# Kernel tuning notes

Hardware: AMD Instinct MI355X
Metric: run time of the kernel (lower is better)

The kernel has to match this reference:

```python
import jax, jax.numpy as jnp
import numpy as np

B, S, T = 4, 1024, 1024
CTX, QIN, C, H = 1024, 1024, 1024, 16
HD = C // H  # per-head channels


def setup_inputs() -> dict:
    key = jax.random.key(0)
    ks = jax.random.split(key, 12)
    s = 0.02
    return {
        "query": jax.random.normal(ks[0], (B, S, QIN), jnp.float32),
        "key": jax.random.normal(ks[1], (B, T, CTX), jnp.float32),
        "value": jax.random.normal(ks[2], (B, T, CTX), jnp.float32),
        "mask": jax.random.randint(ks[3], (B, S, T), 0, 2).astype(bool),
        "Wq": jax.random.normal(ks[4], (C, QIN), jnp.float32) * s,
        "bq": jax.random.normal(ks[5], (C,), jnp.float32) * s,
        "Wk": jax.random.normal(ks[6], (C, CTX), jnp.float32) * s,
        "bk": jax.random.normal(ks[7], (C,), jnp.float32) * s,
        "Wv": jax.random.normal(ks[8], (C, CTX), jnp.float32) * s,
        "bv": jax.random.normal(ks[9], (C,), jnp.float32) * s,
        "Wo": jax.random.normal(ks[10], (C, C), jnp.float32) * s,
        "bo": jax.random.normal(ks[11], (C,), jnp.float32) * s,
    }


def reference(query, key, value, mask, Wq, bq, Wk, bk, Wv, bv, Wo, bo):
    b, s, _ = query.shape
    t = key.shape[1]
    c = Wq.shape[0]
    h, hd = H, c // H
    q = (query @ Wq.T + bq).reshape(b, s, h, hd)
    k = (key @ Wk.T + bk).reshape(b, t, h, hd)
    v = (value @ Wv.T + bv).reshape(b, t, h, hd)
    # [B,H,S,T] scores, scaled by 1/sqrt(head_dim)
    score = jnp.einsum('bshd,bthd->bhst', q, k) * (hd ** -0.5)
    # masked_fill_(~mask[:, None, 0:1], -inf): mask key positions via row 0
    score = jnp.where(mask[:, None, 0:1], score, -jnp.inf)
    weights = jax.nn.softmax(score, axis=-1)
    out = jnp.einsum('bhst,bthd->bshd', weights, v).reshape(b, s, c)
    out = out @ Wo.T + bo
    out = out * mask[..., 0:1].astype(out.dtype)
    return out
```

## Files before the change

### kernel.cpp

```cpp
#include <hip/hip_runtime.h>
#include <stdint.h>

#define Bb  4
#define Ss  1024
#define Tt  1024
#define Cc  1024
#define Hh  16
#define HDd 64
#define Kk  1024

typedef __bf16 bf16;
typedef __bf16 bf16x8 __attribute__((ext_vector_type(8)));
typedef float  f32x4  __attribute__((ext_vector_type(4)));
typedef __attribute__((address_space(1))) uint32_t gu32;
typedef __attribute__((address_space(3))) uint32_t lu32;

__device__ __forceinline__ void load_lds16(const bf16* g, bf16* l) {
    __builtin_amdgcn_global_load_lds((gu32*)g, (lu32*)l, 16, 0, 0);
}

__global__ void cvt8(const float* __restrict__ s0, const float* __restrict__ s1,
                     const float* __restrict__ s2, const float* __restrict__ s3,
                     bf16* __restrict__ d0, bf16* __restrict__ d1,
                     bf16* __restrict__ d2, bf16* __restrict__ d3, int n)
{
    const float* s; bf16* d;
    switch (blockIdx.y) {
        case 0: s = s0; d = d0; break;
        case 1: s = s1; d = d1; break;
        case 2: s = s2; d = d2; break;
        default: s = s3; d = d3; break;
    }
    const int i = (blockIdx.x * blockDim.x + threadIdx.x) * 8;
    if (i >= n) return;
    const float4 a = *(const float4*)(s + i);
    const float4 c = *(const float4*)(s + i + 4);
    bf16x8 o;
    o[0] = (bf16)a.x; o[1] = (bf16)a.y; o[2] = (bf16)a.z; o[3] = (bf16)a.w;
    o[4] = (bf16)c.x; o[5] = (bf16)c.y; o[6] = (bf16)c.z; o[7] = (bf16)c.w;
    *(bf16x8*)(d + i) = o;
}

__device__ __forceinline__ void gemm_mainloop(
    const bf16* __restrict__ A, const bf16* __restrict__ W,
    bf16* As, bf16* Bs, f32x4 acc[4][4])
{
    const int tid  = threadIdx.x;
    const int wid  = tid >> 6;
    const int lane = tid & 63;
    const int l16  = lane & 15;
    const int quad = lane >> 4;
    const int wm   = wid >> 1;
    const int wn   = wid & 1;
    const int lr   = lane >> 2;
    const int lc   = (lane & 3) * 8;
    const bf16* Ab = A + (size_t)blockIdx.x * 128 * Kk;
    const bf16* Wb = W + (size_t)blockIdx.y * 128 * Kk;

    for (int k0 = 0; k0 < Kk; k0 += 32) {
#pragma unroll
        for (int p = 0; p < 2; p++) {
            const int r0 = wid * 32 + p * 16;
            load_lds16(Ab + (size_t)(r0 + lr) * Kk + k0 + lc, As + r0 * 32);
            load_lds16(Wb + (size_t)(r0 + lr) * Kk + k0 + lc, Bs + r0 * 32);
        }
        __syncthreads();
        bf16x8 af[4], bw[4];
#pragma unroll
        for (int i = 0; i < 4; i++)
            af[i] = *(const bf16x8*)(As + (wm * 64 + i * 16 + l16) * 32 + quad * 8);
#pragma unroll
        for (int j = 0; j < 4; j++)
            bw[j] = *(const bf16x8*)(Bs + (wn * 64 + j * 16 + l16) * 32 + quad * 8);
#pragma unroll
        for (int i = 0; i < 4; i++)
#pragma unroll
            for (int j = 0; j < 4; j++)
                acc[i][j] = __builtin_amdgcn_mfma_f32_16x16x32_bf16(af[i], bw[j], acc[i][j], 0, 0, 0);
        __syncthreads();
    }
}

__global__ __launch_bounds__(256)
void gemm_qkv(const bf16* __restrict__ Aq, const bf16* __restrict__ Ak, const bf16* __restrict__ Av,
              const bf16* __restrict__ Wq, const bf16* __restrict__ Wk, const bf16* __restrict__ Wv,
              const float* __restrict__ bq, const float* __restrict__ bk, const float* __restrict__ bv,
              bf16* __restrict__ Oq, bf16* __restrict__ Ok, bf16* __restrict__ Ov)
{
    __shared__ __align__(16) bf16 As[128 * 32];
    __shared__ __align__(16) bf16 Bs[128 * 32];
    const int z = blockIdx.z;
    const bf16*  A    = (z == 0) ? Aq : (z == 1) ? Ak : Av;
    const bf16*  W    = (z == 0) ? Wq : (z == 1) ? Wk : Wv;
    const float* bias = (z == 0) ? bq : (z == 1) ? bk : bv;
    bf16*        O    = (z == 0) ? Oq : (z == 1) ? Ok : Ov;

    f32x4 acc[4][4];
    const f32x4 z4 = {0.f, 0.f, 0.f, 0.f};
#pragma unroll
    for (int i = 0; i < 4; i++)
#pragma unroll
        for (int j = 0; j < 4; j++) acc[i][j] = z4;

    gemm_mainloop(A, W, As, Bs, acc);

    const int tid = threadIdx.x;
    const int wid = tid >> 6, lane = tid & 63;
    const int l16 = lane & 15, quad = lane >> 4;
    const int wm = wid >> 1, wn = wid & 1;
    const int row0 = blockIdx.x * 128 + wm * 64;
    const int col0 = blockIdx.y * 128 + wn * 64;
#pragma unroll
    for (int j = 0; j < 4; j++) {
        const int col = col0 + j * 16 + l16;
        const float bj = bias[col];
        const int h = col >> 6, d = col & 63;
#pragma unroll
        for (int i = 0; i < 4; i++) {
#pragma unroll
            for (int r = 0; r < 4; r++) {
                const int row = row0 + i * 16 + quad * 4 + r;
                const int b = row >> 10, s = row & 1023;
                const bf16 val = (bf16)(acc[i][j][r] + bj);
                if (z == 2) {
                    Ov[((size_t)((b * Hh + h) * HDd + d)) * Tt + s] = val;
                } else {
                    O[((size_t)(b * Hh + h) * Ss + s) * HDd + d] = val;
                }
            }
        }
    }
}

__global__ __launch_bounds__(256)
void gemm_out(const bf16* __restrict__ A, const bf16* __restrict__ W,
              const float* __restrict__ bias, const int* __restrict__ mask,
              float* __restrict__ out)
{
    __shared__ __align__(16) bf16 As[128 * 32];
    __shared__ __align__(16) bf16 Bs[128 * 32];
    f32x4 acc[4][4];
    const f32x4 z4 = {0.f, 0.f, 0.f, 0.f};
#pragma unroll
    for (int i = 0; i < 4; i++)
#pragma unroll
        for (int j = 0; j < 4; j++) acc[i][j] = z4;

    gemm_mainloop(A, W, As, Bs, acc);

    const int tid = threadIdx.x;
    const int wid = tid >> 6, lane = tid & 63;
    const int l16 = lane & 15, quad = lane >> 4;
    const int wm = wid >> 1, wn = wid & 1;
    const int row0 = blockIdx.x * 128 + wm * 64;
    const int col0 = blockIdx.y * 128 + wn * 64;
#pragma unroll
    for (int j = 0; j < 4; j++) {
        const int col = col0 + j * 16 + l16;
        const float bj = bias[col];
#pragma unroll
        for (int i = 0; i < 4; i++) {
#pragma unroll
            for (int r = 0; r < 4; r++) {
                const int row = row0 + i * 16 + quad * 4 + r;
                const float mval = (mask[(size_t)row * Tt] != 0) ? 1.f : 0.f;
                out[(size_t)row * Cc + col] = (acc[i][j][r] + bj) * mval;
            }
        }
    }
}

__global__ __launch_bounds__(256)
void attn(const bf16* __restrict__ Q, const bf16* __restrict__ Kp, const bf16* __restrict__ Vt,
          const int* __restrict__ mask, bf16* __restrict__ X)
{
    __shared__ __align__(16) bf16 Ks[64 * 64];
    __shared__ __align__(16) bf16 Vs[64 * 64];
    __shared__ __align__(16) bf16 Ps[4][16 * 72];
    const int bh = blockIdx.y;
    const int b = bh >> 4, h = bh & 15;
    const int tid = threadIdx.x, wid = tid >> 6, lane = tid & 63;
    const int l16 = lane & 15, quad = lane >> 4;
    const bf16* Qbh = Q  + (size_t)bh * Ss * HDd;
    const bf16* Kbh = Kp + (size_t)bh * Tt * HDd;
    const bf16* Vbh = Vt + (size_t)bh * HDd * Tt;
    const int*  mb  = mask + (size_t)b * Ss * Tt;
    const int q0 = blockIdx.x * 64 + wid * 16;
    bf16* Psw = &Ps[wid][0];

    const bf16x8 qf0 = *(const bf16x8*)(Qbh + (size_t)(q0 + l16) * HDd + quad * 8);
    const bf16x8 qf1 = *(const bf16x8*)(Qbh + (size_t)(q0 + l16) * HDd + 32 + quad * 8);

    float ls[4];
    f32x4 o[4];
    const f32x4 z4 = {0.f, 0.f, 0.f, 0.f};
#pragma unroll
    for (int r = 0; r < 4; r++) ls[r] = 0.f;
#pragma unroll
    for (int dblk = 0; dblk < 4; dblk++) o[dblk] = z4;

    const int srow = lane >> 3;
    const int schk = lane & 7;
    const int sswz = (schk ^ srow) * 8;

    for (int kt = 0; kt < Tt; kt += 64) {
#pragma unroll
        for (int p = 0; p < 2; p++) {
            const int c8 = wid * 2 + p;
            load_lds16(Kbh + (size_t)(kt + c8 * 8 + srow) * HDd + sswz,
                       Ks + c8 * 512);
            load_lds16(Vbh + (size_t)(c8 * 8 + srow) * Tt + kt + sswz,
                       Vs + c8 * 512);
        }
        __syncthreads();

        f32x4 sc[4];
#pragma unroll
        for (int nb = 0; nb < 4; nb++) sc[nb] = z4;
#pragma unroll
        for (int nb = 0; nb < 4; nb++) {
            const bf16* krow = Ks + (nb * 16 + l16) * 64;
            const bf16x8 kf0 = *(const bf16x8*)(krow + ((quad     ^ (l16 & 7)) * 8));
            const bf16x8 kf1 = *(const bf16x8*)(krow + (((4 + quad) ^ (l16 & 7)) * 8));
            sc[nb] = __builtin_amdgcn_mfma_f32_16x16x32_bf16(qf0, kf0, sc[nb], 0, 0, 0);
            sc[nb] = __builtin_amdgcn_mfma_f32_16x16x32_bf16(qf1, kf1, sc[nb], 0, 0, 0);
        }

#pragma unroll
        for (int nb = 0; nb < 4; nb++) {
            const float madd = mb[kt + nb * 16 + l16] ? 0.f : -1e30f;
#pragma unroll
            for (int r = 0; r < 4; r++) {
                const float p = __expf(sc[nb][r] * 0.125f + madd);
                ls[r] += p;
                Psw[(quad * 4 + r) * 72 + nb * 16 + l16] = (bf16)p;
            }
        }

#pragma unroll
        for (int kh = 0; kh < 2; kh++) {
            const bf16x8 pf = *(const bf16x8*)(Psw + l16 * 72 + kh * 32 + quad * 8);
#pragma unroll
            for (int dblk = 0; dblk < 4; dblk++) {
                const bf16x8 vf = *(const bf16x8*)(Vs + (dblk * 16 + l16) * 64 +
                                                   (((kh * 4 + quad) ^ (l16 & 7)) * 8));
                o[dblk] = __builtin_amdgcn_mfma_f32_16x16x32_bf16(pf, vf, o[dblk], 0, 0, 0);
            }
        }
        __syncthreads();
    }

#pragma unroll
    for (int off = 1; off <= 8; off <<= 1)
#pragma unroll
        for (int r = 0; r < 4; r++)
            ls[r] += __shfl_xor(ls[r], off, 64);
    float inv[4];
#pragma unroll
    for (int r = 0; r < 4; r++) inv[r] = 1.f / ls[r];

#pragma unroll
    for (int dblk = 0; dblk < 4; dblk++) {
#pragma unroll
        for (int r = 0; r < 4; r++) {
            const int srow_q = q0 + quad * 4 + r;
            const int d = dblk * 16 + l16;
            X[(size_t)(b * Ss + srow_q) * Cc + h * HDd + d] = (bf16)(o[dblk][r] * inv[r]);
        }
    }
}

extern "C" void kernel_launch(void* const* d_in, const int* in_sizes, int n_in,
                              void* d_out, int out_size, void* d_ws, size_t ws_size,
                              hipStream_t stream)
{
    const float* query = (const float*)d_in[0];
    const float* key   = (const float*)d_in[1];
    const float* value = (const float*)d_in[2];
    const int*   mask  = (const int*)d_in[3];
    const float* Wq = (const float*)d_in[4];
    const float* bq = (const float*)d_in[5];
    const float* Wk = (const float*)d_in[6];
    const float* bk = (const float*)d_in[7];
    const float* Wv = (const float*)d_in[8];
    const float* bv = (const float*)d_in[9];
    const float* Wo = (const float*)d_in[10];
    const float* bo = (const float*)d_in[11];
    float* out = (float*)d_out;

    char* ws = (char*)d_ws;
    const size_t MB = 1024 * 1024;
    bf16* qb  = (bf16*)(ws + 0 * MB);
    bf16* kb  = (bf16*)(ws + 8 * MB);
    bf16* vb  = (bf16*)(ws + 16 * MB);
    bf16* wqb = (bf16*)(ws + 24 * MB);
    bf16* wkb = (bf16*)(ws + 26 * MB);
    bf16* wvb = (bf16*)(ws + 28 * MB);
    bf16* wob = (bf16*)(ws + 30 * MB);
    bf16* Qp  = (bf16*)(ws + 32 * MB);
    bf16* Kpp = (bf16*)(ws + 40 * MB);
    bf16* Vtp = (bf16*)(ws + 48 * MB);
    bf16* Xb  = (bf16*)(ws + 56 * MB);

    cvt8<<<dim3(2048, 3), 256, 0, stream>>>(query, key, value, query,
                                            qb, kb, vb, qb, Bb * Ss * Kk);
    cvt8<<<dim3(512, 4), 256, 0, stream>>>(Wq, Wk, Wv, Wo,
                                           wqb, wkb, wvb, wob, Cc * Kk);
    gemm_qkv<<<dim3(32, 8, 3), 256, 0, stream>>>(qb, kb, vb, wqb, wkb, wvb,
                                                 bq, bk, bv, Qp, Kpp, Vtp);
    attn<<<dim3(16, 64), 256, 0, stream>>>(Qp, Kpp, Vtp, mask, Xb);
    gemm_out<<<dim3(32, 8), 256, 0, stream>>>(Xb, wob, bo, mask, out);
}
```

Baseline: 240.2 us.

## Split attention over key ranges per wave with per-wave pipelined staging and LDS reduction

The attention kernel now gives each wave a 256-key slice of the sequence for all 64 queries of the block, instead of giving each wave 16 queries over all keys. Each wave double-issues its own K/V tile loads into private LDS and uses waitcnt instead of block-wide barriers, so the per-tile __syncthreads goes away. Partial outputs and row sums are combined through LDS at the end, and the results are written as vectorised stores. Softmax uses exp2 with a folded scale, and the mask is hoisted into registers. The two conversion launches are merged into one. Risks are heavier register pressure from 16 accumulator tiles, a large LDS footprint that limits occupancy, and loss of the intra-wave K/V reuse across waves.

```diff
diff --git a/kernel.cpp b/kernel.cpp
--- a/kernel.cpp
+++ b/kernel.cpp
@@ -21,15 +21,22 @@
 
 __global__ void cvt8(const float* __restrict__ s0, const float* __restrict__ s1,
                      const float* __restrict__ s2, const float* __restrict__ s3,
+                     const float* __restrict__ s4, const float* __restrict__ s5,
+                     const float* __restrict__ s6,
                      bf16* __restrict__ d0, bf16* __restrict__ d1,
-                     bf16* __restrict__ d2, bf16* __restrict__ d3, int n)
-{
-    const float* s; bf16* d;
+                     bf16* __restrict__ d2, bf16* __restrict__ d3,
+                     bf16* __restrict__ d4, bf16* __restrict__ d5,
+                     bf16* __restrict__ d6)
+{
+    const float* s; bf16* d; int n;
     switch (blockIdx.y) {
-        case 0: s = s0; d = d0; break;
-        case 1: s = s1; d = d1; break;
-        case 2: s = s2; d = d2; break;
-        default: s = s3; d = d3; break;
+        case 0: s = s0; d = d0; n = Bb * Ss * Kk; break;
+        case 1: s = s1; d = d1; n = Bb * Ss * Kk; break;
+        case 2: s = s2; d = d2; n = Bb * Ss * Kk; break;
+        case 3: s = s3; d = d3; n = Cc * Kk; break;
+        case 4: s = s4; d = d4; n = Cc * Kk; break;
+        case 5: s = s5; d = d5; n = Cc * Kk; break;
+        default: s = s6; d = d6; n = Cc * Kk; break;
     }
     const int i = (blockIdx.x * blockDim.x + threadIdx.x) * 8;
     if (i >= n) return;
@@ -170,104 +177,169 @@
     }
 }
 
-__global__ __launch_bounds__(256)
+#define WAITVM0()   asm volatile("s_waitcnt vmcnt(0)" ::: "memory")
+#define WAITLGKM0() asm volatile("s_waitcnt lgkmcnt(0)" ::: "memory")
+
+__global__ __launch_bounds__(256, 2)
 void attn(const bf16* __restrict__ Q, const bf16* __restrict__ Kp, const bf16* __restrict__ Vt,
           const int* __restrict__ mask, bf16* __restrict__ X)
 {
-    __shared__ __align__(16) bf16 Ks[64 * 64];
-    __shared__ __align__(16) bf16 Vs[64 * 64];
-    __shared__ __align__(16) bf16 Ps[4][16 * 72];
+    __shared__ __align__(16) char smem_raw[70656];
+    bf16* smem = (bf16*)smem_raw;
     const int bh = blockIdx.y;
     const int b = bh >> 4, h = bh & 15;
     const int tid = threadIdx.x, wid = tid >> 6, lane = tid & 63;
     const int l16 = lane & 15, quad = lane >> 4;
-    const bf16* Qbh = Q  + (size_t)bh * Ss * HDd;
-    const bf16* Kbh = Kp + (size_t)bh * Tt * HDd;
-    const bf16* Vbh = Vt + (size_t)bh * HDd * Tt;
-    const int*  mb  = mask + (size_t)b * Ss * Tt;
-    const int q0 = blockIdx.x * 64 + wid * 16;
-    bf16* Psw = &Ps[wid][0];
-
-    const bf16x8 qf0 = *(const bf16x8*)(Qbh + (size_t)(q0 + l16) * HDd + quad * 8);
-    const bf16x8 qf1 = *(const bf16x8*)(Qbh + (size_t)(q0 + l16) * HDd + 32 + quad * 8);
-
-    float ls[4];
-    f32x4 o[4];
+    const int q0 = blockIdx.x * 64;
+
+    const bf16* Qbh  = Q  + (size_t)bh * Ss * HDd;
+    const bf16* KbhW = Kp + (size_t)bh * Tt * HDd + (size_t)(wid * 256) * HDd;
+    const bf16* VbhW = Vt + (size_t)bh * HDd * Tt + wid * 256;
+    const int*  mbW  = mask + (size_t)b * Ss * Tt + wid * 256;
+
+    bf16* wslot = smem + wid * 5376;
+    bf16* kb = wslot;
+    bf16* vb = wslot + 2048;
+    bf16* Pbuf[2] = { wslot + 4096, wslot + 4736 };
+
+    const int r8  = lane >> 3;
+    const int sw8 = ((lane & 7) ^ (r8 & 7)) * 8;
+    const int r4  = lane >> 2;
+    const int sw4 = ((lane & 3) ^ (r4 & 3)) * 8;
+
+#define STAGE(ii) do { \
+    _Pragma("unroll") \
+    for (int c = 0; c < 4; ++c) \
+        load_lds16(KbhW + (size_t)((ii) * 32 + c * 8 + r8) * HDd + sw8, kb + c * 512); \
+    _Pragma("unroll") \
+    for (int c = 0; c < 4; ++c) \
+        load_lds16(VbhW + (size_t)(c * 16 + r4) * Tt + (ii) * 32 + sw4, vb + c * 512); \
+} while (0)
+
+    bf16x8 qf[4][2];
+#pragma unroll
+    for (int mi = 0; mi < 4; ++mi)
+#pragma unroll
+        for (int kh = 0; kh < 2; ++kh)
+            qf[mi][kh] = *(const bf16x8*)(Qbh + (size_t)(q0 + mi * 16 + l16) * HDd + kh * 32 + quad * 8);
+
+    float madd[16];
+#pragma unroll
+    for (int j = 0; j < 16; ++j)
+        madd[j] = mbW[j * 16 + l16] ? 0.f : -1e30f;
+
     const f32x4 z4 = {0.f, 0.f, 0.f, 0.f};
-#pragma unroll
-    for (int r = 0; r < 4; r++) ls[r] = 0.f;
-#pragma unroll
-    for (int dblk = 0; dblk < 4; dblk++) o[dblk] = z4;
-
-    const int srow = lane >> 3;
-    const int schk = lane & 7;
-    const int sswz = (schk ^ srow) * 8;
-
-    for (int kt = 0; kt < Tt; kt += 64) {
-#pragma unroll
-        for (int p = 0; p < 2; p++) {
-            const int c8 = wid * 2 + p;
-            load_lds16(Kbh + (size_t)(kt + c8 * 8 + srow) * HDd + sswz,
-                       Ks + c8 * 512);
-            load_lds16(Vbh + (size_t)(c8 * 8 + srow) * Tt + kt + sswz,
-                       Vs + c8 * 512);
+    f32x4 o[4][4];
+    float ls[4][4];
+#pragma unroll
+    for (int mi = 0; mi < 4; ++mi) {
+#pragma unroll
+        for (int dblk = 0; dblk < 4; ++dblk) o[mi][dblk] = z4;
+#pragma unroll
+        for (int r = 0; r < 4; ++r) ls[mi][r] = 0.f;
+    }
+
+    const float C2 = 0.18033688f;
+
+    STAGE(0);
+#pragma unroll
+    for (int i = 0; i < 8; ++i) {
+        WAITVM0();
+        bf16x8 kf[2][2], vf[4];
+#pragma unroll
+        for (int nb = 0; nb < 2; ++nb)
+#pragma unroll
+            for (int kh = 0; kh < 2; ++kh)
+                kf[nb][kh] = *(const bf16x8*)(kb + (nb * 16 + l16) * 64 +
+                                              (((kh * 4 + quad) ^ (l16 & 7)) * 8));
+#pragma unroll
+        for (int dblk = 0; dblk < 4; ++dblk)
+            vf[dblk] = *(const bf16x8*)(vb + (dblk * 16 + l16) * 32 +
+                                        ((quad ^ (l16 & 3)) * 8));
+        WAITLGKM0();
+        if (i < 7) STAGE(i + 1);
+
+#define QKEXP(mi, pb) do { \
+    f32x4 s0 = z4, s1 = z4; \
+    s0 = __builtin_amdgcn_mfma_f32_16x16x32_bf16(qf[mi][0], kf[0][0], s0, 0, 0, 0); \
+    s0 = __builtin_amdgcn_mfma_f32_16x16x32_bf16(qf[mi][1], kf[0][1], s0, 0, 0, 0); \
+    s1 = __builtin_amdgcn_mfma_f32_16x16x32_bf16(qf[mi][0], kf[1][0], s1, 0, 0, 0); \
+    s1 = __builtin_amdgcn_mfma_f32_16x16x32_bf16(qf[mi][1], kf[1][1], s1, 0, 0, 0); \
+    _Pragma("unroll") \
+    for (int r = 0; r < 4; ++r) { \
+        const float p0 = exp2f(s0[r] * C2 + madd[i * 2 + 0]); \
+        const float p1 = exp2f(s1[r] * C2 + madd[i * 2 + 1]); \
+        ls[mi][r] += p0 + p1; \
+        (pb)[(quad * 4 + r) * 40 + l16]      = (bf16)p0; \
+        (pb)[(quad * 4 + r) * 40 + 16 + l16] = (bf16)p1; \
+    } \
+} while (0)
+
+        QKEXP(0, Pbuf[0]);
+#pragma unroll
+        for (int mi = 0; mi < 4; ++mi) {
+            if (mi == 0) QKEXP(1, Pbuf[1]);
+            if (mi == 1) QKEXP(2, Pbuf[0]);
+            if (mi == 2) QKEXP(3, Pbuf[1]);
+            const bf16x8 pf = *(const bf16x8*)(Pbuf[mi & 1] + l16 * 40 + quad * 8);
+#pragma unroll
+            for (int dblk = 0; dblk < 4; ++dblk)
+                o[mi][dblk] = __builtin_amdgcn_mfma_f32_16x16x32_bf16(pf, vf[dblk], o[mi][dblk], 0, 0, 0);
         }
-        __syncthreads();
-
-        f32x4 sc[4];
-#pragma unroll
-        for (int nb = 0; nb < 4; nb++) sc[nb] = z4;
-#pragma unroll
-        for (int nb = 0; nb < 4; nb++) {
-            const bf16* krow = Ks + (nb * 16 + l16) * 64;
-            const bf16x8 kf0 = *(const bf16x8*)(krow + ((quad     ^ (l16 & 7)) * 8));
-            const bf16x8 kf1 = *(const bf16x8*)(krow + (((4 + quad) ^ (l16 & 7)) * 8));
-            sc[nb] = __builtin_amdgcn_mfma_f32_16x16x32_bf16(qf0, kf0, sc[nb], 0, 0, 0);
-            sc[nb] = __builtin_amdgcn_mfma_f32_16x16x32_bf16(qf1, kf1, sc[nb], 0, 0, 0);
-        }
-
-#pragma unroll
-        for (int nb = 0; nb < 4; nb++) {
-            const float madd = mb[kt + nb * 16 + l16] ? 0.f : -1e30f;
-#pragma unroll
-            for (int r = 0; r < 4; r++) {
-                const float p = __expf(sc[nb][r] * 0.125f + madd);
-                ls[r] += p;
-                Psw[(quad * 4 + r) * 72 + nb * 16 + l16] = (bf16)p;
-            }
-        }
-
-#pragma unroll
-        for (int kh = 0; kh < 2; kh++) {
-            const bf16x8 pf = *(const bf16x8*)(Psw + l16 * 72 + kh * 32 + quad * 8);
-#pragma unroll
-            for (int dblk = 0; dblk < 4; dblk++) {
-                const bf16x8 vf = *(const bf16x8*)(Vs + (dblk * 16 + l16) * 64 +
-                                                   (((kh * 4 + quad) ^ (l16 & 7)) * 8));
-                o[dblk] = __builtin_amdgcn_mfma_f32_16x16x32_bf16(pf, vf, o[dblk], 0, 0, 0);
-            }
-        }
-        __syncthreads();
-    }
+#undef QKEXP
+    }
+#undef STAGE
 
 #pragma unroll
     for (int off = 1; off <= 8; off <<= 1)
 #pragma unroll
-        for (int r = 0; r < 4; r++)
-            ls[r] += __shfl_xor(ls[r], off, 64);
-    float inv[4];
-#pragma unroll
-    for (int r = 0; r < 4; r++) inv[r] = 1.f / ls[r];
-
-#pragma unroll
-    for (int dblk = 0; dblk < 4; dblk++) {
-#pragma unroll
-        for (int r = 0; r < 4; r++) {
-            const int srow_q = q0 + quad * 4 + r;
-            const int d = dblk * 16 + l16;
-            X[(size_t)(b * Ss + srow_q) * Cc + h * HDd + d] = (bf16)(o[dblk][r] * inv[r]);
-        }
-    }
+        for (int mi = 0; mi < 4; ++mi)
+#pragma unroll
+            for (int r = 0; r < 4; ++r)
+                ls[mi][r] += __shfl_xor(ls[mi][r], off, 64);
+
+    __syncthreads();
+    float* Om = (float*)smem + wid * 4416;
+#pragma unroll
+    for (int mi = 0; mi < 4; ++mi)
+#pragma unroll
+        for (int dblk = 0; dblk < 4; ++dblk)
+#pragma unroll
+            for (int r = 0; r < 4; ++r)
+                Om[(mi * 16 + quad * 4 + r) * 68 + dblk * 16 + l16] = o[mi][dblk][r];
+    if (l16 == 0) {
+#pragma unroll
+        for (int mi = 0; mi < 4; ++mi)
+#pragma unroll
+            for (int r = 0; r < 4; ++r)
+                Om[4352 + mi * 16 + quad * 4 + r] = ls[mi][r];
+    }
+    __syncthreads();
+
+    const int rl = wid * 16 + l16;
+    f32x4 a[4] = { z4, z4, z4, z4 };
+    float lt = 0.f;
+#pragma unroll
+    for (int u = 0; u < 4; ++u) {
+        const float* Ou = (const float*)smem + u * 4416;
+#pragma unroll
+        for (int e = 0; e < 4; ++e)
+            a[e] += *(const f32x4*)(Ou + rl * 68 + quad * 16 + e * 4);
+        lt += Ou[4352 + rl];
+    }
+    const float inv = 1.f / lt;
+
+    bf16x8 w0, w1;
+#pragma unroll
+    for (int c = 0; c < 4; ++c) {
+        w0[c]     = (bf16)(a[0][c] * inv);
+        w0[4 + c] = (bf16)(a[1][c] * inv);
+        w1[c]     = (bf16)(a[2][c] * inv);
+        w1[4 + c] = (bf16)(a[3][c] * inv);
+    }
+    bf16* Xrow = X + (size_t)(b * Ss + q0 + rl) * Cc + h * HDd + quad * 16;
+    *(bf16x8*)(Xrow)     = w0;
+    *(bf16x8*)(Xrow + 8) = w1;
 }
 
 extern "C" void kernel_launch(void* const* d_in, const int* in_sizes, int n_in,
@@ -302,10 +374,8 @@
     bf16* Vtp = (bf16*)(ws + 48 * MB);
     bf16* Xb  = (bf16*)(ws + 56 * MB);
 
-    cvt8<<<dim3(2048, 3), 256, 0, stream>>>(query, key, value, query,
-                                            qb, kb, vb, qb, Bb * Ss * Kk);
-    cvt8<<<dim3(512, 4), 256, 0, stream>>>(Wq, Wk, Wv, Wo,
-                                           wqb, wkb, wvb, wob, Cc * Kk);
+    cvt8<<<dim3(2048, 7), 256, 0, stream>>>(query, key, value, Wq, Wk, Wv, Wo,
+                                            qb, kb, vb, wqb, wkb, wvb, wob);
     gemm_qkv<<<dim3(32, 8, 3), 256, 0, stream>>>(qb, kb, vb, wqb, wkb, wvb,
                                                  bq, bk, bv, Qp, Kpp, Vtp);
     attn<<<dim3(16, 64), 256, 0, stream>>>(Qp, Kpp, Vtp, mask, Xb);
```

Measured after the change: 264.9 us. 1.1x slower.

## Double-buffer K/V tiles in attention and merge conversion launches

Applied to the files above, without the earlier changes.

The attention kernel now keeps two LDS buffers for its K and V tiles. It issues the async global-to-LDS load for the next tile right after a single barrier, so the copy overlaps with the current tile's MFMA and softmax work, and the trailing barrier is dropped. The two fp32-to-bf16 conversion launches are merged into one grid with seven slices, each carrying its own length. This saves a kernel launch, but the weight slices launch many blocks that exit immediately, and the doubled LDS use may lower occupancy.

```diff
diff --git a/kernel.cpp b/kernel.cpp
--- a/kernel.cpp
+++ b/kernel.cpp
@@ -21,15 +21,22 @@
 
 __global__ void cvt8(const float* __restrict__ s0, const float* __restrict__ s1,
                      const float* __restrict__ s2, const float* __restrict__ s3,
+                     const float* __restrict__ s4, const float* __restrict__ s5,
+                     const float* __restrict__ s6,
                      bf16* __restrict__ d0, bf16* __restrict__ d1,
-                     bf16* __restrict__ d2, bf16* __restrict__ d3, int n)
-{
-    const float* s; bf16* d;
+                     bf16* __restrict__ d2, bf16* __restrict__ d3,
+                     bf16* __restrict__ d4, bf16* __restrict__ d5,
+                     bf16* __restrict__ d6)
+{
+    const float* s; bf16* d; int n;
     switch (blockIdx.y) {
-        case 0: s = s0; d = d0; break;
-        case 1: s = s1; d = d1; break;
-        case 2: s = s2; d = d2; break;
-        default: s = s3; d = d3; break;
+        case 0: s = s0; d = d0; n = Bb * Ss * Kk; break;
+        case 1: s = s1; d = d1; n = Bb * Ss * Kk; break;
+        case 2: s = s2; d = d2; n = Bb * Ss * Kk; break;
+        case 3: s = s3; d = d3; n = Cc * Kk; break;
+        case 4: s = s4; d = d4; n = Cc * Kk; break;
+        case 5: s = s5; d = d5; n = Cc * Kk; break;
+        default: s = s6; d = d6; n = Cc * Kk; break;
     }
     const int i = (blockIdx.x * blockDim.x + threadIdx.x) * 8;
     if (i >= n) return;
@@ -174,8 +181,8 @@
 void attn(const bf16* __restrict__ Q, const bf16* __restrict__ Kp, const bf16* __restrict__ Vt,
           const int* __restrict__ mask, bf16* __restrict__ X)
 {
-    __shared__ __align__(16) bf16 Ks[64 * 64];
-    __shared__ __align__(16) bf16 Vs[64 * 64];
+    __shared__ __align__(16) bf16 Ks[2][64 * 64];
+    __shared__ __align__(16) bf16 Vs[2][64 * 64];
     __shared__ __align__(16) bf16 Ps[4][16 * 72];
     const int bh = blockIdx.y;
     const int b = bh >> 4, h = bh & 15;
@@ -203,24 +210,31 @@
     const int schk = lane & 7;
     const int sswz = (schk ^ srow) * 8;
 
-    for (int kt = 0; kt < Tt; kt += 64) {
-#pragma unroll
-        for (int p = 0; p < 2; p++) {
-            const int c8 = wid * 2 + p;
-            load_lds16(Kbh + (size_t)(kt + c8 * 8 + srow) * HDd + sswz,
-                       Ks + c8 * 512);
-            load_lds16(Vbh + (size_t)(c8 * 8 + srow) * Tt + kt + sswz,
-                       Vs + c8 * 512);
-        }
+#define STAGE(it, buf) do { \
+    _Pragma("unroll") \
+    for (int p = 0; p < 2; p++) { \
+        const int c8 = wid * 2 + p; \
+        load_lds16(Kbh + (size_t)((it) * 64 + c8 * 8 + srow) * HDd + sswz, \
+                   Ks[buf] + c8 * 512); \
+        load_lds16(Vbh + (size_t)(c8 * 8 + srow) * Tt + (it) * 64 + sswz, \
+                   Vs[buf] + c8 * 512); \
+    } \
+} while (0)
+
+    STAGE(0, 0);
+    for (int it = 0; it < 16; ++it) {
+        const int cur = it & 1;
+        const int kt = it * 64;
         __syncthreads();
+        if (it < 15) STAGE(it + 1, cur ^ 1);
 
         f32x4 sc[4];
 #pragma unroll
         for (int nb = 0; nb < 4; nb++) sc[nb] = z4;
 #pragma unroll
         for (int nb = 0; nb < 4; nb++) {
-            const bf16* krow = Ks + (nb * 16 + l16) * 64;
-            const bf16x8 kf0 = *(const bf16x8*)(krow + ((quad     ^ (l16 & 7)) * 8));
+            const bf16* krow = Ks[cur] + (nb * 16 + l16) * 64;
+            const bf16x8 kf0 = *(const bf16x8*)(krow + ((quad       ^ (l16 & 7)) * 8));
             const bf16x8 kf1 = *(const bf16x8*)(krow + (((4 + quad) ^ (l16 & 7)) * 8));
             sc[nb] = __builtin_amdgcn_mfma_f32_16x16x32_bf16(qf0, kf0, sc[nb], 0, 0, 0);
             sc[nb] = __builtin_amdgcn_mfma_f32_16x16x32_bf16(qf1, kf1, sc[nb], 0, 0, 0);
@@ -242,13 +256,13 @@
             const bf16x8 pf = *(const bf16x8*)(Psw + l16 * 72 + kh * 32 + quad * 8);
 #pragma unroll
             for (int dblk = 0; dblk < 4; dblk++) {
-                const bf16x8 vf = *(const bf16x8*)(Vs + (dblk * 16 + l16) * 64 +
+                const bf16x8 vf = *(const bf16x8*)(Vs[cur] + (dblk * 16 + l16) * 64 +
                                                    (((kh * 4 + quad) ^ (l16 & 7)) * 8));
                 o[dblk] = __builtin_amdgcn_mfma_f32_16x16x32_bf16(pf, vf, o[dblk], 0, 0, 0);
             }
         }
-        __syncthreads();
-    }
+    }
+#undef STAGE
 
 #pragma unroll
     for (int off = 1; off <= 8; off <<= 1)
@@ -302,10 +316,8 @@
     bf16* Vtp = (bf16*)(ws + 48 * MB);
     bf16* Xb  = (bf16*)(ws + 56 * MB);
 
-    cvt8<<<dim3(2048, 3), 256, 0, stream>>>(query, key, value, query,
-                                            qb, kb, vb, qb, Bb * Ss * Kk);
-    cvt8<<<dim3(512, 4), 256, 0, stream>>>(Wq, Wk, Wv, Wo,
-                                           wqb, wkb, wvb, wob, Cc * Kk);
+    cvt8<<<dim3(2048, 7), 256, 0, stream>>>(query, key, value, Wq, Wk, Wv, Wo,
+                                            qb, kb, vb, wqb, wkb, wvb, wob);
     gemm_qkv<<<dim3(32, 8, 3), 256, 0, stream>>>(qb, kb, vb, wqb, wkb, wvb,
                                                  bq, bk, bv, Qp, Kpp, Vtp);
     attn<<<dim3(16, 64), 256, 0, stream>>>(Qp, Kpp, Vtp, mask, Xb);
```

After: 243.9 us. No clear change (+1.6%).

## Deepen GEMM K-step to 64 with XOR-swizzled LDS, smaller out-proj tiles, merged convert

Applied to the files above, without the earlier changes.

The GEMM main loop now stages 64-wide K slices per barrier pair instead of 32, halving the number of syncs, and stores them in LDS with an XOR swizzle to avoid bank conflicts on the fragment reads. The output projection switches to 64x128 tiles, doubling its grid to 512 blocks so more CUs are busy. The two fp32-to-bf16 conversion launches are merged into one launch, with the weight slices using early exit for the unused blocks. LDS per block doubles, which may lower occupancy, and the weight blocks of the merged convert launch are mostly idle.

```diff
diff --git a/kernel.cpp b/kernel.cpp
--- a/kernel.cpp
+++ b/kernel.cpp
@@ -21,15 +21,22 @@
 
 __global__ void cvt8(const float* __restrict__ s0, const float* __restrict__ s1,
                      const float* __restrict__ s2, const float* __restrict__ s3,
+                     const float* __restrict__ s4, const float* __restrict__ s5,
+                     const float* __restrict__ s6,
                      bf16* __restrict__ d0, bf16* __restrict__ d1,
-                     bf16* __restrict__ d2, bf16* __restrict__ d3, int n)
-{
-    const float* s; bf16* d;
+                     bf16* __restrict__ d2, bf16* __restrict__ d3,
+                     bf16* __restrict__ d4, bf16* __restrict__ d5,
+                     bf16* __restrict__ d6)
+{
+    const float* s; bf16* d; int n;
     switch (blockIdx.y) {
-        case 0: s = s0; d = d0; break;
-        case 1: s = s1; d = d1; break;
-        case 2: s = s2; d = d2; break;
-        default: s = s3; d = d3; break;
+        case 0: s = s0; d = d0; n = Bb * Ss * Kk; break;
+        case 1: s = s1; d = d1; n = Bb * Ss * Kk; break;
+        case 2: s = s2; d = d2; n = Bb * Ss * Kk; break;
+        case 3: s = s3; d = d3; n = Cc * Kk; break;
+        case 4: s = s4; d = d4; n = Cc * Kk; break;
+        case 5: s = s5; d = d5; n = Cc * Kk; break;
+        default: s = s6; d = d6; n = Cc * Kk; break;
     }
     const int i = (blockIdx.x * blockDim.x + threadIdx.x) * 8;
     if (i >= n) return;
@@ -41,8 +48,8 @@
     *(bf16x8*)(d + i) = o;
 }
 
-__device__ __forceinline__ void gemm_mainloop(
-    const bf16* __restrict__ A, const bf16* __restrict__ W,
+__device__ __forceinline__ void mainloop_128(
+    const bf16* __restrict__ Ab, const bf16* __restrict__ Wb,
     bf16* As, bf16* Bs, f32x4 acc[4][4])
 {
     const int tid  = threadIdx.x;
@@ -52,31 +59,81 @@
     const int quad = lane >> 4;
     const int wm   = wid >> 1;
     const int wn   = wid & 1;
-    const int lr   = lane >> 2;
-    const int lc   = (lane & 3) * 8;
-    const bf16* Ab = A + (size_t)blockIdx.x * 128 * Kk;
-    const bf16* Wb = W + (size_t)blockIdx.y * 128 * Kk;
-
-    for (int k0 = 0; k0 < Kk; k0 += 32) {
+    const int r8   = lane >> 3;
+    const int ssw  = ((lane & 7) ^ r8) * 8;
+
+    for (int k0 = 0; k0 < Kk; k0 += 64) {
+#pragma unroll
+        for (int p = 0; p < 4; p++) {
+            const int rb = wid * 32 + p * 8;
+            load_lds16(Ab + (size_t)(rb + r8) * Kk + k0 + ssw, As + rb * 64);
+            load_lds16(Wb + (size_t)(rb + r8) * Kk + k0 + ssw, Bs + rb * 64);
+        }
+        __syncthreads();
+#pragma unroll
+        for (int kh = 0; kh < 2; kh++) {
+            bf16x8 af[4], bw[4];
+#pragma unroll
+            for (int i = 0; i < 4; i++)
+                af[i] = *(const bf16x8*)(As + (wm * 64 + i * 16 + l16) * 64 +
+                                         (((kh * 4 + quad) ^ (l16 & 7)) * 8));
+#pragma unroll
+            for (int j = 0; j < 4; j++)
+                bw[j] = *(const bf16x8*)(Bs + (wn * 64 + j * 16 + l16) * 64 +
+                                         (((kh * 4 + quad) ^ (l16 & 7)) * 8));
+#pragma unroll
+            for (int i = 0; i < 4; i++)
+#pragma unroll
+                for (int j = 0; j < 4; j++)
+                    acc[i][j] = __builtin_amdgcn_mfma_f32_16x16x32_bf16(af[i], bw[j], acc[i][j], 0, 0, 0);
+        }
+        __syncthreads();
+    }
+}
+
+__device__ __forceinline__ void mainloop_64(
+    const bf16* __restrict__ Ab, const bf16* __restrict__ Wb,
+    bf16* As, bf16* Bs, f32x4 acc[2][4])
+{
+    const int tid  = threadIdx.x;
+    const int wid  = tid >> 6;
+    const int lane = tid & 63;
+    const int l16  = lane & 15;
+    const int quad = lane >> 4;
+    const int wm   = wid >> 1;
+    const int wn   = wid & 1;
+    const int r8   = lane >> 3;
+    const int ssw  = ((lane & 7) ^ r8) * 8;
+
+    for (int k0 = 0; k0 < Kk; k0 += 64) {
 #pragma unroll
         for (int p = 0; p < 2; p++) {
-            const int r0 = wid * 32 + p * 16;
-            load_lds16(Ab + (size_t)(r0 + lr) * Kk + k0 + lc, As + r0 * 32);
-            load_lds16(Wb + (size_t)(r0 + lr) * Kk + k0 + lc, Bs + r0 * 32);
-        }
-        __syncthreads();
-        bf16x8 af[4], bw[4];
-#pragma unroll
-        for (int i = 0; i < 4; i++)
-            af[i] = *(const bf16x8*)(As + (wm * 64 + i * 16 + l16) * 32 + quad * 8);
-#pragma unroll
-        for (int j = 0; j < 4; j++)
-            bw[j] = *(const bf16x8*)(Bs + (wn * 64 + j * 16 + l16) * 32 + quad * 8);
-#pragma unroll
-        for (int i = 0; i < 4; i++)
+            const int rb = wid * 16 + p * 8;
+            load_lds16(Ab + (size_t)(rb + r8) * Kk + k0 + ssw, As + rb * 64);
+        }
+#pragma unroll
+        for (int p = 0; p < 4; p++) {
+            const int rb = wid * 32 + p * 8;
+            load_lds16(Wb + (size_t)(rb + r8) * Kk + k0 + ssw, Bs + rb * 64);
+        }
+        __syncthreads();
+#pragma unroll
+        for (int kh = 0; kh < 2; kh++) {
+            bf16x8 af[2], bw[4];
+#pragma unroll
+            for (int i = 0; i < 2; i++)
+                af[i] = *(const bf16x8*)(As + (wm * 32 + i * 16 + l16) * 64 +
+                                         (((kh * 4 + quad) ^ (l16 & 7)) * 8));
 #pragma unroll
             for (int j = 0; j < 4; j++)
-                acc[i][j] = __builtin_amdgcn_mfma_f32_16x16x32_bf16(af[i], bw[j], acc[i][j], 0, 0, 0);
+                bw[j] = *(const bf16x8*)(Bs + (wn * 64 + j * 16 + l16) * 64 +
+                                         (((kh * 4 + quad) ^ (l16 & 7)) * 8));
+#pragma unroll
+            for (int i = 0; i < 2; i++)
+#pragma unroll
+                for (int j = 0; j < 4; j++)
+                    acc[i][j] = __builtin_amdgcn_mfma_f32_16x16x32_bf16(af[i], bw[j], acc[i][j], 0, 0, 0);
+        }
         __syncthreads();
     }
 }
@@ -87,8 +144,8 @@
               const float* __restrict__ bq, const float* __restrict__ bk, const float* __restrict__ bv,
               bf16* __restrict__ Oq, bf16* __restrict__ Ok, bf16* __restrict__ Ov)
 {
-    __shared__ __align__(16) bf16 As[128 * 32];
-    __shared__ __align__(16) bf16 Bs[128 * 32];
+    __shared__ __align__(16) bf16 As[128 * 64];
+    __shared__ __align__(16) bf16 Bs[128 * 64];
     const int z = blockIdx.z;
     const bf16*  A    = (z == 0) ? Aq : (z == 1) ? Ak : Av;
     const bf16*  W    = (z == 0) ? Wq : (z == 1) ? Wk : Wv;
@@ -102,7 +159,8 @@
 #pragma unroll
         for (int j = 0; j < 4; j++) acc[i][j] = z4;
 
-    gemm_mainloop(A, W, As, Bs, acc);
+    mainloop_128(A + (size_t)blockIdx.x * 128 * Kk,
+                 W + (size_t)blockIdx.y * 128 * Kk, As, Bs, acc);
 
     const int tid = threadIdx.x;
     const int wid = tid >> 6, lane = tid & 63;
@@ -137,29 +195,30 @@
               const float* __restrict__ bias, const int* __restrict__ mask,
               float* __restrict__ out)
 {
-    __shared__ __align__(16) bf16 As[128 * 32];
-    __shared__ __align__(16) bf16 Bs[128 * 32];
-    f32x4 acc[4][4];
+    __shared__ __align__(16) bf16 As[64 * 64];
+    __shared__ __align__(16) bf16 Bs[128 * 64];
+    f32x4 acc[2][4];
     const f32x4 z4 = {0.f, 0.f, 0.f, 0.f};
 #pragma unroll
-    for (int i = 0; i < 4; i++)
+    for (int i = 0; i < 2; i++)
 #pragma unroll
         for (int j = 0; j < 4; j++) acc[i][j] = z4;
 
-    gemm_mainloop(A, W, As, Bs, acc);
+    mainloop_64(A + (size_t)blockIdx.x * 64 * Kk,
+                W + (size_t)blockIdx.y * 128 * Kk, As, Bs, acc);
 
     const int tid = threadIdx.x;
     const int wid = tid >> 6, lane = tid & 63;
     const int l16 = lane & 15, quad = lane >> 4;
     const int wm = wid >> 1, wn = wid & 1;
-    const int row0 = blockIdx.x * 128 + wm * 64;
+    const int row0 = blockIdx.x * 64 + wm * 32;
     const int col0 = blockIdx.y * 128 + wn * 64;
 #pragma unroll
     for (int j = 0; j < 4; j++) {
         const int col = col0 + j * 16 + l16;
         const float bj = bias[col];
 #pragma unroll
-        for (int i = 0; i < 4; i++) {
+        for (int i = 0; i < 2; i++) {
 #pragma unroll
             for (int r = 0; r < 4; r++) {
                 const int row = row0 + i * 16 + quad * 4 + r;
@@ -302,12 +361,10 @@
     bf16* Vtp = (bf16*)(ws + 48 * MB);
     bf16* Xb  = (bf16*)(ws + 56 * MB);
 
-    cvt8<<<dim3(2048, 3), 256, 0, stream>>>(query, key, value, query,
-                                            qb, kb, vb, qb, Bb * Ss * Kk);
-    cvt8<<<dim3(512, 4), 256, 0, stream>>>(Wq, Wk, Wv, Wo,
-                                           wqb, wkb, wvb, wob, Cc * Kk);
+    cvt8<<<dim3(2048, 7), 256, 0, stream>>>(query, key, value, Wq, Wk, Wv, Wo,
+                                            qb, kb, vb, wqb, wkb, wvb, wob);
     gemm_qkv<<<dim3(32, 8, 3), 256, 0, stream>>>(qb, kb, vb, wqb, wkb, wvb,
                                                  bq, bk, bv, Qp, Kpp, Vtp);
     attn<<<dim3(16, 64), 256, 0, stream>>>(Qp, Kpp, Vtp, mask, Xb);
-    gemm_out<<<dim3(32, 8), 256, 0, stream>>>(Xb, wob, bo, mask, out);
-}
+    gemm_out<<<dim3(64, 8), 256, 0, stream>>>(Xb, wob, bo, mask, out);
+}
```

Result: no change. 241.5 us (+0.5%).
